# Performance work log

Measured on AMD Instinct MI355X. Metric: run time of the kernel, lower is better.

Reference implementation:

```python
import jax, jax.numpy as jnp
import numpy as np

B, S, D, H = 2, 2048, 1024, 16
HD = D // H  # head_dim = 64


def setup_inputs() -> dict:
    key = jax.random.key(0)
    ks = jax.random.split(key, 5)
    scale = 1.0 / np.sqrt(D)
    return {
        "x": jax.random.normal(ks[0], (B, S, D), dtype=jnp.float32),
        "attention_mask": jnp.zeros((B, 1, 1, S), dtype=jnp.float32),
        "Wq": jax.random.normal(ks[1], (D, D), dtype=jnp.float32) * scale,
        "Wk": jax.random.normal(ks[2], (D, D), dtype=jnp.float32) * scale,
        "Wv": jax.random.normal(ks[3], (D, D), dtype=jnp.float32) * scale,
        "Wo": jax.random.normal(ks[4], (D, D), dtype=jnp.float32) * scale,
    }


def reference(x, attention_mask, Wq, Wk, Wv, Wo):
    # nn.Linear applies x @ W.T; weights here stored as [out, in]
    q = jnp.einsum("bsd,ed->bse", x, Wq).reshape(B, S, H, HD).transpose(0, 2, 1, 3)
    k = jnp.einsum("bsd,ed->bse", x, Wk).reshape(B, S, H, HD).transpose(0, 2, 1, 3)
    v = jnp.einsum("bsd,ed->bse", x, Wv).reshape(B, S, H, HD).transpose(0, 2, 1, 3)
    scores = jnp.einsum("bhqd,bhkd->bhqk", q, k) / jnp.sqrt(jnp.float32(HD))
    scores = scores + attention_mask  # additive mask, broadcasts [B,1,1,S]
    attn = jax.nn.softmax(scores, axis=-1)  # dropout p=0 (eval) -> identity
    ctx = jnp.einsum("bhqk,bhkd->bhqd", attn, v)
    ctx = ctx.transpose(0, 2, 1, 3).reshape(B, S, D)
    out = jnp.einsum("bsd,ed->bse", ctx, Wo)
    return out
```

## Files before the change

kernel.cpp:

```cpp
#include <hip/hip_runtime.h>
#include <hip/hip_bf16.h>
#include <cstdint>
#include <cstddef>


#define B_  2
#define S_  2048
#define D_  1024
#define H_  16
#define HD_ 64

typedef __bf16 bf16x8 __attribute__((ext_vector_type(8)));
typedef __bf16 bf16x4 __attribute__((ext_vector_type(4)));
typedef float  f32x4  __attribute__((ext_vector_type(4)));

__device__ __forceinline__ void async16(const __bf16* g, const __bf16* l) {
  __builtin_amdgcn_global_load_lds(
      (const __attribute__((address_space(1))) void*)(uintptr_t)g,
      (__attribute__((address_space(3))) void*)(uint32_t)(uintptr_t)l,
      16, 0, 0);
}

__device__ __forceinline__ unsigned cvt_pk_bf16(float lo, float hi) {
  unsigned r;
  asm("v_cvt_pk_bf16_f32 %0, %1, %2" : "=v"(r) : "v"(lo), "v"(hi));
  return r;
}

__global__ __launch_bounds__(256) void cvt_all(const float* __restrict__ x,
    const float* __restrict__ wq, const float* __restrict__ wk,
    const float* __restrict__ wv, const float* __restrict__ wo,
    __bf16* __restrict__ xb, __bf16* __restrict__ wqb, __bf16* __restrict__ wkb,
    __bf16* __restrict__ wvb, __bf16* __restrict__ wob) {
  const int sel = blockIdx.y;
  const float* src; __bf16* dst; int n;
  if      (sel == 0) { src = x;  dst = xb;  n = B_ * S_ * D_; }
  else if (sel == 1) { src = wq; dst = wqb; n = D_ * D_; }
  else if (sel == 2) { src = wk; dst = wkb; n = D_ * D_; }
  else if (sel == 3) { src = wv; dst = wvb; n = D_ * D_; }
  else               { src = wo; dst = wob; n = D_ * D_; }
  for (int i = blockIdx.x * 256 + threadIdx.x; i * 4 < n; i += gridDim.x * 256) {
    const float4 v = *(const float4*)(src + (size_t)i * 4);
    bf16x4 o;
    o[0] = (__bf16)v.x; o[1] = (__bf16)v.y; o[2] = (__bf16)v.z; o[3] = (__bf16)v.w;
    *(bf16x4*)(dst + (size_t)i * 4) = o;
  }
}

__global__ __launch_bounds__(256) void qkv_gemm(const __bf16* __restrict__ xb,
                                                const __bf16* __restrict__ wqkv,
                                                __bf16* __restrict__ qkv) {
  __shared__ __align__(16) char smem[32768];
  __bf16* As = (__bf16*)smem;
  __bf16* Bs = (__bf16*)(smem + 16384);
  __bf16* cs = (__bf16*)smem;

  const int lin = blockIdx.y * 24 + blockIdx.x;
  const int xcd = lin & 7, slot = lin >> 3;
  const int mi = xcd >> 2, ni = xcd & 3;
  const int mB = mi * 16 + slot / 6;
  const int nB = ni * 6  + slot % 6;
  const int m0  = mB * 128;
  const int sel = nB >> 3;
  const int n0s = (nB & 7) * 128;
  const int n0w = nB * 128;
  constexpr int K = D_, N = D_;
  constexpr size_t NTE = (size_t)B_ * S_ * D_;

  const int tid  = threadIdx.x, lane = tid & 63, wave = tid >> 6;
  const int l15  = lane & 15,   quad = lane >> 4;
  const int wr   = wave >> 1,   wc   = wave & 1;
  const int ebase = wave * 2048 + lane * 8;

  f32x4 acc[4][4] = {};
  for (int k0 = 0; k0 < K; k0 += 64) {
#pragma unroll
    for (int i = 0; i < 4; ++i) {
      const int e = ebase + i * 512;
      const int row = e >> 6, col = e & 63;
      async16(xb   + (size_t)(m0  + row) * K + k0 + col, As + (wave * 4 + i) * 512);
      async16(wqkv + (size_t)(n0w + row) * K + k0 + col, Bs + (wave * 4 + i) * 512);
    }
    __syncthreads();
#pragma unroll
    for (int kk = 0; kk < 2; ++kk) {
      bf16x8 af[4], bfv[4];
#pragma unroll
      for (int rt = 0; rt < 4; ++rt)
        af[rt] = *(const bf16x8*)(As + (wr * 64 + rt * 16 + l15) * 64 + kk * 32 + quad * 8);
#pragma unroll
      for (int ct = 0; ct < 4; ++ct)
        bfv[ct] = *(const bf16x8*)(Bs + (wc * 64 + ct * 16 + l15) * 64 + kk * 32 + quad * 8);
#pragma unroll
      for (int rt = 0; rt < 4; ++rt)
#pragma unroll
        for (int ct = 0; ct < 4; ++ct)
          acc[rt][ct] = __builtin_amdgcn_mfma_f32_16x16x32_bf16(af[rt], bfv[ct], acc[rt][ct], 0, 0, 0);
    }
    __syncthreads();
  }

  const int b  = m0 >> 11;
  const int s0 = m0 & (S_ - 1);
  __bf16* vtb = qkv + 2 * NTE;
#pragma unroll
  for (int pass = 0; pass < 2; ++pass) {
    __syncthreads();
    if (wr == pass) {
#pragma unroll
      for (int rt = 0; rt < 4; ++rt)
#pragma unroll
        for (int ct = 0; ct < 4; ++ct)
#pragma unroll
          for (int r = 0; r < 4; ++r)
            cs[(rt * 16 + quad * 4 + r) * 136 + wc * 64 + ct * 16 + l15] =
                (__bf16)acc[rt][ct][r];
    }
    __syncthreads();
    if (sel < 2) {
      __bf16* C = qkv + (size_t)sel * NTE;
      const int cc = tid & 15, rr = tid >> 4;
#pragma unroll
      for (int p2 = 0; p2 < 4; ++p2) {
        const int row = p2 * 16 + rr;
        const bf16x8 v = *(const bf16x8*)(cs + row * 136 + cc * 8);
        *(bf16x8*)(C + (size_t)(m0 + pass * 64 + row) * N + n0s + cc * 8) = v;
      }
    } else {
      const int e_loc = tid >> 1, sh = (tid & 1) * 32;
      __bf16* dst = vtb + (size_t)(b * 1024 + n0s + e_loc) * S_ + s0 + pass * 64 + sh;
#pragma unroll
      for (int p2 = 0; p2 < 4; ++p2) {
        bf16x8 v;
#pragma unroll
        for (int j = 0; j < 8; ++j)
          v[j] = cs[(sh + p2 * 8 + j) * 136 + e_loc];
        *(bf16x8*)(dst + p2 * 8) = v;
      }
    }
  }
}

__global__ __launch_bounds__(256) void o_gemm(const __bf16* __restrict__ cb,
                                              const __bf16* __restrict__ wo,
                                              float* __restrict__ out) {
  __shared__ __align__(16) __bf16 As[64 * 64];
  __shared__ __align__(16) __bf16 Bs[128 * 64];
  const int lin = blockIdx.y * 8 + blockIdx.x;
  const int xcd = lin & 7, slot = lin >> 3;
  const int mi = xcd >> 1, ni = xcd & 1;
  const int mB = mi * 16 + (slot >> 2);
  const int nB = ni * 4  + (slot & 3);
  const int m0 = mB * 64, n0 = nB * 128;
  constexpr int K = D_, N = D_;
  const int tid  = threadIdx.x, lane = tid & 63, wave = tid >> 6;
  const int l15  = lane & 15,   quad = lane >> 4;
  const int wr   = wave >> 1,   wc   = wave & 1;

  f32x4 acc[2][4] = {};
  for (int k0 = 0; k0 < K; k0 += 64) {
#pragma unroll
    for (int i = 0; i < 2; ++i) {
      const int e = i * 2048 + wave * 512 + (lane & 63) * 8;
      const int row = e >> 6, col = e & 63;
      async16(cb + (size_t)(m0 + row) * K + k0 + col, As + i * 2048 + wave * 512);
    }
#pragma unroll
    for (int j = 0; j < 4; ++j) {
      const int e = j * 2048 + wave * 512 + (lane & 63) * 8;
      const int row = e >> 6, col = e & 63;
      async16(wo + (size_t)(n0 + row) * K + k0 + col, Bs + j * 2048 + wave * 512);
    }
    __syncthreads();
#pragma unroll
    for (int kk = 0; kk < 2; ++kk) {
      bf16x8 af[2], bfv[4];
#pragma unroll
      for (int rt = 0; rt < 2; ++rt)
        af[rt] = *(const bf16x8*)(As + (wr * 32 + rt * 16 + l15) * 64 + kk * 32 + quad * 8);
#pragma unroll
      for (int ct = 0; ct < 4; ++ct)
        bfv[ct] = *(const bf16x8*)(Bs + (wc * 64 + ct * 16 + l15) * 64 + kk * 32 + quad * 8);
#pragma unroll
      for (int rt = 0; rt < 2; ++rt)
#pragma unroll
        for (int ct = 0; ct < 4; ++ct)
          acc[rt][ct] = __builtin_amdgcn_mfma_f32_16x16x32_bf16(af[rt], bfv[ct], acc[rt][ct], 0, 0, 0);
    }
    __syncthreads();
  }
#pragma unroll
  for (int rt = 0; rt < 2; ++rt)
#pragma unroll
    for (int ct = 0; ct < 4; ++ct)
#pragma unroll
      for (int r = 0; r < 4; ++r) {
        const int row = m0 + wr * 32 + rt * 16 + quad * 4 + r;
        const int col = n0 + wc * 64 + ct * 16 + l15;
        out[(size_t)row * N + col] = acc[rt][ct][r];
      }
}

__global__ __launch_bounds__(512, 4) void attn2(const __bf16* __restrict__ Q,
                                                const __bf16* __restrict__ K,
                                                const __bf16* __restrict__ Vt,
                                                const float* __restrict__ mask,
                                                __bf16* __restrict__ O) {
  constexpr int LKT = 72, LVT = 136;
  __shared__ __align__(16) __bf16 kt[2][128 * LKT];
  __shared__ __align__(16) __bf16 vt[2][64 * LVT];
  __shared__ __align__(16) float  mfull[S_];

  const int tid  = threadIdx.x, lane = tid & 63, wave = tid >> 6;
  const int l15  = lane & 15,   quad = lane >> 4;
  const int lin = blockIdx.z * 256 + blockIdx.y * 16 + blockIdx.x;
  const int swz = (lin & 7) * 64 + (lin >> 3);
  const int b = swz >> 8, h = (swz >> 4) & 15, q0 = (swz & 15) * 128;
  const size_t base   = (size_t)b * S_ * D_ + h * HD_;
  const size_t vtbase = (size_t)(b * H_ + h) * HD_ * S_;
  const int qw = q0 + wave * 16;
  constexpr float LOG2E = 1.44269504088896340736f;
  constexpr float SC    = 0.125f * LOG2E;
  constexpr int  NT     = S_ / 128;

  const int idx0 = tid,        kr0 = idx0 >> 3, kc0 = (idx0 & 7) * 8;
  const int idx1 = 512 + tid,  kr1 = idx1 >> 3, kc1 = (idx1 & 7) * 8;
  const int vr0 = idx0 >> 4, vc0 = (idx0 & 15) * 8;
  const int vr1 = idx1 >> 4, vc1 = (idx1 & 15) * 8;

  bf16x8 qf[2];
#pragma unroll
  for (int kb = 0; kb < 2; ++kb)
    qf[kb] = *(const bf16x8*)(Q + base + (size_t)(qw + l15) * D_ + kb * 32 + quad * 8);

  bf16x8 ones;
#pragma unroll
  for (int j = 0; j < 8; ++j) ones[j] = (__bf16)1.0f;

  float m_run = -1e30f;
  f32x4 oacc[4] = {};
  f32x4 lacc   = {};

  bf16x8 rk0, rk1, rv0, rv1;
  rk0 = *(const bf16x8*)(K + base + (size_t)kr0 * D_ + kc0);
  rk1 = *(const bf16x8*)(K + base + (size_t)kr1 * D_ + kc1);
  rv0 = *(const bf16x8*)(Vt + vtbase + (size_t)vr0 * S_ + vc0);
  rv1 = *(const bf16x8*)(Vt + vtbase + (size_t)vr1 * S_ + vc1);
#pragma unroll
  for (int i = 0; i < S_ / 512; ++i)
    mfull[i * 512 + tid] = mask[(size_t)b * S_ + i * 512 + tid] * LOG2E;
  *(bf16x8*)(&kt[0][kr0 * LKT + kc0]) = rk0;
  *(bf16x8*)(&kt[0][kr1 * LKT + kc1]) = rk1;
  *(bf16x8*)(&vt[0][vr0 * LVT + vc0]) = rv0;
  *(bf16x8*)(&vt[0][vr1 * LVT + vc1]) = rv1;
  __syncthreads();

  for (int t = 0; t < NT; ++t) {
    const int cur = t & 1;
    const int t0  = t * 128;
    const __bf16* ktb = &kt[cur][0];
    const __bf16* vtb = &vt[cur][0];

    if (t + 1 < NT) {
      const int tn = t0 + 128;
      rk0 = *(const bf16x8*)(K + base + (size_t)(tn + kr0) * D_ + kc0);
      rk1 = *(const bf16x8*)(K + base + (size_t)(tn + kr1) * D_ + kc1);
      rv0 = *(const bf16x8*)(Vt + vtbase + (size_t)vr0 * S_ + tn + vc0);
      rv1 = *(const bf16x8*)(Vt + vtbase + (size_t)vr1 * S_ + tn + vc1);
    }

    f32x4 sacc[8] = {};
    __builtin_amdgcn_s_setprio(1);
#pragma unroll
    for (int kti = 0; kti < 8; ++kti) {
      const __bf16* kr = ktb + (kti * 16 + l15) * LKT + quad * 8;
      const bf16x8 a0 = *(const bf16x8*)(kr);
      const bf16x8 a1 = *(const bf16x8*)(kr + 32);
      sacc[kti] = __builtin_amdgcn_mfma_f32_16x16x32_bf16(a0, qf[0], sacc[kti], 0, 0, 0);
      sacc[kti] = __builtin_amdgcn_mfma_f32_16x16x32_bf16(a1, qf[1], sacc[kti], 0, 0, 0);
    }
    __builtin_amdgcn_s_setprio(0);

    f32x4 tm4;
#pragma unroll
    for (int r = 0; r < 4; ++r) tm4[r] = -1e30f;
#pragma unroll
    for (int kti = 0; kti < 8; ++kti) {
      const f32x4 mv = *(const f32x4*)(mfull + t0 + kti * 16 + quad * 4);
#pragma unroll
      for (int r = 0; r < 4; ++r) {
        sacc[kti][r] = sacc[kti][r] * SC + mv[r];
        tm4[r] = fmaxf(tm4[r], sacc[kti][r]);
      }
    }
    float tm = fmaxf(fmaxf(tm4[0], tm4[1]), fmaxf(tm4[2], tm4[3]));
    tm = fmaxf(tm, __shfl_xor(tm, 16));
    tm = fmaxf(tm, __shfl_xor(tm, 32));

    if (!__all(tm <= m_run + 8.f)) {
      const float mnew  = fmaxf(m_run, tm);
      const float alpha = __builtin_amdgcn_exp2f(m_run - mnew);
      m_run = mnew;
#pragma unroll
      for (int r = 0; r < 4; ++r) {
        const float aR = __shfl(alpha, quad * 4 + r);
        lacc[r] *= aR;
#pragma unroll
        for (int nt = 0; nt < 4; ++nt) oacc[nt][r] *= aR;
      }
    }

#pragma unroll
    for (int kb = 0; kb < 4; ++kb) {
      unsigned dd[2][2];
#pragma unroll
      for (int kk = 0; kk < 2; ++kk) {
        const int kti = 2 * kb + kk;
        float p[4];
#pragma unroll
        for (int r = 0; r < 4; ++r)
          p[r] = __builtin_amdgcn_exp2f(sacc[kti][r] - m_run);
        dd[kk][0] = cvt_pk_bf16(p[0], p[1]);
        dd[kk][1] = cvt_pk_bf16(p[2], p[3]);
      }
      unsigned a0 = dd[0][0], b0 = dd[1][0], a1 = dd[0][1], b1 = dd[1][1];
      asm("v_permlane32_swap_b32 %0, %1" : "+v"(a0), "+v"(b0));
      asm("v_permlane16_swap_b32 %0, %1" : "+v"(a0), "+v"(b0));
      asm("v_permlane32_swap_b32 %0, %1" : "+v"(a1), "+v"(b1));
      asm("v_permlane16_swap_b32 %0, %1" : "+v"(a1), "+v"(b1));
      union { unsigned u[4]; bf16x8 v; } pw;
      pw.u[0] = a0; pw.u[1] = a1; pw.u[2] = b0; pw.u[3] = b1;
      const bf16x8 pa = pw.v;
      __builtin_amdgcn_s_setprio(1);
      lacc = __builtin_amdgcn_mfma_f32_16x16x32_bf16(pa, ones, lacc, 0, 0, 0);
#pragma unroll
      for (int nt = 0; nt < 4; ++nt) {
        const bf16x8 vf = *(const bf16x8*)(vtb + (nt * 16 + l15) * LVT + kb * 32 + quad * 8);
        oacc[nt] = __builtin_amdgcn_mfma_f32_16x16x32_bf16(pa, vf, oacc[nt], 0, 0, 0);
      }
      __builtin_amdgcn_s_setprio(0);
    }

    __syncthreads();
    if (t + 1 < NT) {
      const int nxt = cur ^ 1;
      *(bf16x8*)(&kt[nxt][kr0 * LKT + kc0]) = rk0;
      *(bf16x8*)(&kt[nxt][kr1 * LKT + kc1]) = rk1;
      *(bf16x8*)(&vt[nxt][vr0 * LVT + vc0]) = rv0;
      *(bf16x8*)(&vt[nxt][vr1 * LVT + vc1]) = rv1;
    }
    __syncthreads();
  }

#pragma unroll
  for (int r = 0; r < 4; ++r) {
    const float inv = 1.0f / lacc[r];
    const int row = qw + quad * 4 + r;
#pragma unroll
    for (int nt = 0; nt < 4; ++nt)
      O[base + (size_t)row * D_ + nt * 16 + l15] = (__bf16)(oacc[nt][r] * inv);
  }
}

extern "C" void kernel_launch(void* const* d_in, const int* in_sizes, int n_in,
                              void* d_out, int out_size, void* d_ws, size_t ws_size,
                              hipStream_t stream) {
  const float* x    = (const float*)d_in[0];
  const float* mask = (const float*)d_in[1];
  const float* Wq   = (const float*)d_in[2];
  const float* Wk   = (const float*)d_in[3];
  const float* Wv   = (const float*)d_in[4];
  const float* Wo   = (const float*)d_in[5];

  char* ws = (char*)d_ws;
  const size_t MB = 1ull << 20;
  const size_t NT = (size_t)B_ * S_ * D_;
  __bf16* xb  = (__bf16*)(ws);
  __bf16* wqb = (__bf16*)(ws + 8 * MB);
  __bf16* wkb = (__bf16*)(ws + 10 * MB);
  __bf16* wvb = (__bf16*)(ws + 12 * MB);
  __bf16* wob = (__bf16*)(ws + 14 * MB);
  __bf16* qkv = (__bf16*)(ws + 16 * MB);
  __bf16* qb  = qkv;
  __bf16* kb  = qkv + NT;
  __bf16* vtb = qkv + 2 * NT;
  __bf16* cb  = xb;

  cvt_all<<<dim3(1024, 5), 256, 0, stream>>>(x, Wq, Wk, Wv, Wo, xb, wqb, wkb, wvb, wob);
  qkv_gemm<<<dim3(24, 32), 256, 0, stream>>>(xb, wqb, qkv);
  attn2<<<dim3(S_ / 128, H_, B_), 512, 0, stream>>>(qb, kb, vtb, mask, cb);
  o_gemm<<<dim3(8, 64), 256, 0, stream>>>(cb, wob, (float*)d_out);
}
```

Baseline: 210.3 us.

## Double-buffer LDS in both GEMMs, enlarge o_gemm tile, and deepen attention K/V prefetch

The QKV and output GEMMs now double-buffer LDS (64KB) so async global-to-LDS loads for the next K tile are issued while the current tile is multiplied, which cuts one barrier per iteration. o_gemm moves to 128x128 tiles on half as many blocks, improving reuse per block but lowering block count. The attention kernel drops its XCD block swizzle and pipelines K/V two tiles ahead, writing the next tile to the alternate LDS buffer at the start of each iteration and removing a barrier. The larger LDS use may reduce occupancy, and the deeper register prefetch adds register pressure.

```diff
diff --git a/kernel.cpp b/kernel.cpp
--- a/kernel.cpp
+++ b/kernel.cpp
@@ -50,9 +50,7 @@
 __global__ __launch_bounds__(256) void qkv_gemm(const __bf16* __restrict__ xb,
                                                 const __bf16* __restrict__ wqkv,
                                                 __bf16* __restrict__ qkv) {
-  __shared__ __align__(16) char smem[32768];
-  __bf16* As = (__bf16*)smem;
-  __bf16* Bs = (__bf16*)(smem + 16384);
+  __shared__ __align__(16) char smem[65536];
   __bf16* cs = (__bf16*)smem;
 
   const int lin = blockIdx.y * 24 + blockIdx.x;
@@ -73,15 +71,36 @@
   const int ebase = wave * 2048 + lane * 8;
 
   f32x4 acc[4][4] = {};
-  for (int k0 = 0; k0 < K; k0 += 64) {
+
+  {
+    __bf16* As = (__bf16*)(smem);
+    __bf16* Bs = (__bf16*)(smem + 16384);
 #pragma unroll
     for (int i = 0; i < 4; ++i) {
       const int e = ebase + i * 512;
       const int row = e >> 6, col = e & 63;
-      async16(xb   + (size_t)(m0  + row) * K + k0 + col, As + (wave * 4 + i) * 512);
-      async16(wqkv + (size_t)(n0w + row) * K + k0 + col, Bs + (wave * 4 + i) * 512);
-    }
-    __syncthreads();
+      async16(xb   + (size_t)(m0  + row) * K + col, As + (wave * 4 + i) * 512);
+      async16(wqkv + (size_t)(n0w + row) * K + col, Bs + (wave * 4 + i) * 512);
+    }
+  }
+  __syncthreads();
+
+  for (int t = 0; t < K / 64; ++t) {
+    const int cur = t & 1;
+    if (t + 1 < K / 64) {
+      const int k0 = (t + 1) * 64;
+      __bf16* As = (__bf16*)(smem + (cur ^ 1) * 32768);
+      __bf16* Bs = (__bf16*)(smem + (cur ^ 1) * 32768 + 16384);
+#pragma unroll
+      for (int i = 0; i < 4; ++i) {
+        const int e = ebase + i * 512;
+        const int row = e >> 6, col = e & 63;
+        async16(xb   + (size_t)(m0  + row) * K + k0 + col, As + (wave * 4 + i) * 512);
+        async16(wqkv + (size_t)(n0w + row) * K + k0 + col, Bs + (wave * 4 + i) * 512);
+      }
+    }
+    const __bf16* As = (const __bf16*)(smem + cur * 32768);
+    const __bf16* Bs = (const __bf16*)(smem + cur * 32768 + 16384);
 #pragma unroll
     for (int kk = 0; kk < 2; ++kk) {
       bf16x8 af[4], bfv[4];
@@ -144,45 +163,60 @@
 __global__ __launch_bounds__(256) void o_gemm(const __bf16* __restrict__ cb,
                                               const __bf16* __restrict__ wo,
                                               float* __restrict__ out) {
-  __shared__ __align__(16) __bf16 As[64 * 64];
-  __shared__ __align__(16) __bf16 Bs[128 * 64];
+  __shared__ __align__(16) char smem[65536];
   const int lin = blockIdx.y * 8 + blockIdx.x;
   const int xcd = lin & 7, slot = lin >> 3;
   const int mi = xcd >> 1, ni = xcd & 1;
-  const int mB = mi * 16 + (slot >> 2);
-  const int nB = ni * 4  + (slot & 3);
-  const int m0 = mB * 64, n0 = nB * 128;
+  const int mB = mi * 8 + (slot >> 2);
+  const int nB = ni * 4 + (slot & 3);
+  const int m0 = mB * 128, n0 = nB * 128;
   constexpr int K = D_, N = D_;
   const int tid  = threadIdx.x, lane = tid & 63, wave = tid >> 6;
   const int l15  = lane & 15,   quad = lane >> 4;
   const int wr   = wave >> 1,   wc   = wave & 1;
-
-  f32x4 acc[2][4] = {};
-  for (int k0 = 0; k0 < K; k0 += 64) {
-#pragma unroll
-    for (int i = 0; i < 2; ++i) {
-      const int e = i * 2048 + wave * 512 + (lane & 63) * 8;
+  const int ebase = wave * 2048 + lane * 8;
+
+  f32x4 acc[4][4] = {};
+  {
+    __bf16* As = (__bf16*)(smem);
+    __bf16* Bs = (__bf16*)(smem + 16384);
+#pragma unroll
+    for (int i = 0; i < 4; ++i) {
+      const int e = ebase + i * 512;
       const int row = e >> 6, col = e & 63;
-      async16(cb + (size_t)(m0 + row) * K + k0 + col, As + i * 2048 + wave * 512);
-    }
-#pragma unroll
-    for (int j = 0; j < 4; ++j) {
-      const int e = j * 2048 + wave * 512 + (lane & 63) * 8;
-      const int row = e >> 6, col = e & 63;
-      async16(wo + (size_t)(n0 + row) * K + k0 + col, Bs + j * 2048 + wave * 512);
-    }
-    __syncthreads();
+      async16(cb + (size_t)(m0 + row) * K + col, As + (wave * 4 + i) * 512);
+      async16(wo + (size_t)(n0 + row) * K + col, Bs + (wave * 4 + i) * 512);
+    }
+  }
+  __syncthreads();
+
+  for (int t = 0; t < K / 64; ++t) {
+    const int cur = t & 1;
+    if (t + 1 < K / 64) {
+      const int k0 = (t + 1) * 64;
+      __bf16* As = (__bf16*)(smem + (cur ^ 1) * 32768);
+      __bf16* Bs = (__bf16*)(smem + (cur ^ 1) * 32768 + 16384);
+#pragma unroll
+      for (int i = 0; i < 4; ++i) {
+        const int e = ebase + i * 512;
+        const int row = e >> 6, col = e & 63;
+        async16(cb + (size_t)(m0 + row) * K + k0 + col, As + (wave * 4 + i) * 512);
+        async16(wo + (size_t)(n0 + row) * K + k0 + col, Bs + (wave * 4 + i) * 512);
+      }
+    }
+    const __bf16* As = (const __bf16*)(smem + cur * 32768);
+    const __bf16* Bs = (const __bf16*)(smem + cur * 32768 + 16384);
 #pragma unroll
     for (int kk = 0; kk < 2; ++kk) {
-      bf16x8 af[2], bfv[4];
-#pragma unroll
-      for (int rt = 0; rt < 2; ++rt)
-        af[rt] = *(const bf16x8*)(As + (wr * 32 + rt * 16 + l15) * 64 + kk * 32 + quad * 8);
+      bf16x8 af[4], bfv[4];
+#pragma unroll
+      for (int rt = 0; rt < 4; ++rt)
+        af[rt] = *(const bf16x8*)(As + (wr * 64 + rt * 16 + l15) * 64 + kk * 32 + quad * 8);
 #pragma unroll
       for (int ct = 0; ct < 4; ++ct)
         bfv[ct] = *(const bf16x8*)(Bs + (wc * 64 + ct * 16 + l15) * 64 + kk * 32 + quad * 8);
 #pragma unroll
-      for (int rt = 0; rt < 2; ++rt)
+      for (int rt = 0; rt < 4; ++rt)
 #pragma unroll
         for (int ct = 0; ct < 4; ++ct)
           acc[rt][ct] = __builtin_amdgcn_mfma_f32_16x16x32_bf16(af[rt], bfv[ct], acc[rt][ct], 0, 0, 0);
@@ -190,12 +224,12 @@
     __syncthreads();
   }
 #pragma unroll
-  for (int rt = 0; rt < 2; ++rt)
+  for (int rt = 0; rt < 4; ++rt)
 #pragma unroll
     for (int ct = 0; ct < 4; ++ct)
 #pragma unroll
       for (int r = 0; r < 4; ++r) {
-        const int row = m0 + wr * 32 + rt * 16 + quad * 4 + r;
+        const int row = m0 + wr * 64 + rt * 16 + quad * 4 + r;
         const int col = n0 + wc * 64 + ct * 16 + l15;
         out[(size_t)row * N + col] = acc[rt][ct][r];
       }
@@ -213,9 +247,7 @@
 
   const int tid  = threadIdx.x, lane = tid & 63, wave = tid >> 6;
   const int l15  = lane & 15,   quad = lane >> 4;
-  const int lin = blockIdx.z * 256 + blockIdx.y * 16 + blockIdx.x;
-  const int swz = (lin & 7) * 64 + (lin >> 3);
-  const int b = swz >> 8, h = (swz >> 4) & 15, q0 = (swz & 15) * 128;
+  const int b = blockIdx.z, h = blockIdx.y, q0 = blockIdx.x * 128;
   const size_t base   = (size_t)b * S_ * D_ + h * HD_;
   const size_t vtbase = (size_t)(b * H_ + h) * HD_ * S_;
   const int qw = q0 + wave * 16;
@@ -253,6 +285,12 @@
   *(bf16x8*)(&kt[0][kr1 * LKT + kc1]) = rk1;
   *(bf16x8*)(&vt[0][vr0 * LVT + vc0]) = rv0;
   *(bf16x8*)(&vt[0][vr1 * LVT + vc1]) = rv1;
+  if (NT > 1) {
+    rk0 = *(const bf16x8*)(K + base + (size_t)(128 + kr0) * D_ + kc0);
+    rk1 = *(const bf16x8*)(K + base + (size_t)(128 + kr1) * D_ + kc1);
+    rv0 = *(const bf16x8*)(Vt + vtbase + (size_t)vr0 * S_ + 128 + vc0);
+    rv1 = *(const bf16x8*)(Vt + vtbase + (size_t)vr1 * S_ + 128 + vc1);
+  }
   __syncthreads();
 
   for (int t = 0; t < NT; ++t) {
@@ -262,7 +300,14 @@
     const __bf16* vtb = &vt[cur][0];
 
     if (t + 1 < NT) {
-      const int tn = t0 + 128;
+      const int nxt = cur ^ 1;
+      *(bf16x8*)(&kt[nxt][kr0 * LKT + kc0]) = rk0;
+      *(bf16x8*)(&kt[nxt][kr1 * LKT + kc1]) = rk1;
+      *(bf16x8*)(&vt[nxt][vr0 * LVT + vc0]) = rv0;
+      *(bf16x8*)(&vt[nxt][vr1 * LVT + vc1]) = rv1;
+    }
+    if (t + 2 < NT) {
+      const int tn = t0 + 256;
       rk0 = *(const bf16x8*)(K + base + (size_t)(tn + kr0) * D_ + kc0);
       rk1 = *(const bf16x8*)(K + base + (size_t)(tn + kr1) * D_ + kc1);
       rv0 = *(const bf16x8*)(Vt + vtbase + (size_t)vr0 * S_ + tn + vc0);
@@ -341,14 +386,6 @@
       __builtin_amdgcn_s_setprio(0);
     }
 
-    __syncthreads();
-    if (t + 1 < NT) {
-      const int nxt = cur ^ 1;
-      *(bf16x8*)(&kt[nxt][kr0 * LKT + kc0]) = rk0;
-      *(bf16x8*)(&kt[nxt][kr1 * LKT + kc1]) = rk1;
-      *(bf16x8*)(&vt[nxt][vr0 * LVT + vc0]) = rv0;
-      *(bf16x8*)(&vt[nxt][vr1 * LVT + vc1]) = rv1;
-    }
     __syncthreads();
   }
 
@@ -389,5 +426,5 @@
   cvt_all<<<dim3(1024, 5), 256, 0, stream>>>(x, Wq, Wk, Wv, Wo, xb, wqb, wkb, wvb, wob);
   qkv_gemm<<<dim3(24, 32), 256, 0, stream>>>(xb, wqb, qkv);
   attn2<<<dim3(S_ / 128, H_, B_), 512, 0, stream>>>(qb, kb, vtb, mask, cb);
-  o_gemm<<<dim3(8, 64), 256, 0, stream>>>(cb, wob, (float*)d_out);
-}
+  o_gemm<<<dim3(8, 32), 256, 0, stream>>>(cb, wob, (float*)d_out);
+}
```

Result: faster. 198.8 us (-5.5%).
